# Performance work log

Hardware: AMD Instinct MI355X
Metric: run time of the kernel (lower is better)

Reference implementation:

```python
import jax, jax.numpy as jnp
import numpy as np

TEMPERATURE = 0.04


def _d3tod2(t):
    # 'c h w -> (h w) c'
    c, h, w = t.shape
    return jnp.transpose(t, (1, 2, 0)).reshape(h * w, c)


def setup_inputs() -> dict:
    key = jax.random.key(0)
    k1, k2 = jax.random.split(key)
    B, C, H, W = 4, 128, 96, 96
    # scale 0.05 keeps dot/temperature in a numerically sane range for exp
    x = jax.random.normal(k1, (B, C, H, W), dtype=jnp.float32) * 0.05
    label = jax.random.randint(k2, (B, 1, H, W), 0, 3, dtype=jnp.int32)
    return {"x": x, "label": label}


def reference(x, label):
    B, C, H, W = x.shape
    hw = H * W
    feat_1 = _d3tod2(x[0])                     # [HW, C]
    feat_2 = _d3tod2(x[1])                     # [HW, C]
    gt1 = label[0, 0].reshape(hw)              # [HW]
    gt2 = label[1, 0].reshape(hw)              # [HW]
    sim = jnp.exp(jnp.matmul(feat_1, feat_2.T) / TEMPERATURE)  # [HW, HW]
    mask = gt1[:, None] == gt2[None, :]        # [HW, HW] label-equality
    pos_sum = jnp.sum(jnp.where(mask, sim, jnp.zeros((), sim.dtype)))
    total_sum = jnp.sum(sim)
    loss = -jnp.log(pos_sum / total_sum) / (hw * hw)
    return loss
```

## Files before the change

kernel.cpp:

```cpp
#include <hip/hip_runtime.h>
#include <hip/hip_bf16.h>

#define HW 9216
#define CDIM 128
#define BM 128
#define BN 64
#define JT 8
#define GRID_I (HW / BM)
#define GRID_J (HW / (BN * JT))
#define NPART (GRID_I * GRID_J * 4)
#define LDP (CDIM + 8)

using bf16 = __hip_bfloat16;
typedef __attribute__((ext_vector_type(4))) float f32x4;
typedef __attribute__((ext_vector_type(8))) short s16x8;

#define EXP_SCALE 36.067376022224085f

#if __has_builtin(__builtin_amdgcn_exp2f)
#define FEXP2(x) __builtin_amdgcn_exp2f(x)
#else
#define FEXP2(x) exp2f(x)
#endif

__global__ __launch_bounds__(256) void prep_kernel(const float* __restrict__ x,
                                                   bf16* __restrict__ feat) {
    __shared__ float tile[64][65];
    const float* xs = x + (size_t)blockIdx.z * CDIM * HW;
    bf16* fs = feat + (size_t)blockIdx.z * HW * CDIM;
    float scale = (blockIdx.z == 0) ? EXP_SCALE : 1.0f;

    int p0 = blockIdx.x * 64;
    int c0 = blockIdx.y * 64;
    int t  = threadIdx.x;

    int pc = t & 63;
    int cr = t >> 6;
#pragma unroll
    for (int i = 0; i < 16; ++i) {
        int cl = cr + i * 4;
        tile[cl][pc] = xs[(size_t)(c0 + cl) * HW + p0 + pc];
    }
    __syncthreads();

    int cc = t & 63;
    int pr = t >> 6;
#pragma unroll
    for (int i = 0; i < 16; ++i) {
        int pl = pr + i * 4;
        fs[(size_t)(p0 + pl) * CDIM + c0 + cc] = __float2bfloat16(tile[cc][pl] * scale);
    }
}

__global__ __launch_bounds__(256) void simsum_kernel(const bf16* __restrict__ feat1,
                                                     const bf16* __restrict__ feat2,
                                                     const int* __restrict__ label,
                                                     float* __restrict__ partials) {
    __shared__ bf16 Bs[2][BN][LDP];
    __shared__ int  labs[JT * BN];
    __shared__ float red[8];

    int t    = threadIdx.x;
    int w    = t >> 6;
    int lane = t & 63;
    int lr   = lane & 15;
    int kg   = lane >> 4;

    int i0 = blockIdx.x * BM;
    int jb = blockIdx.y * (JT * BN);

    s16x8 af[2][4];
#pragma unroll
    for (int m = 0; m < 2; ++m) {
        const bf16* arow = &feat1[(size_t)(i0 + w * 32 + m * 16 + lr) * CDIM + kg * 8];
#pragma unroll
        for (int ks = 0; ks < 4; ++ks)
            af[m][ks] = *(const s16x8*)(arow + ks * 32);
    }

    int g1v[2][4];
#pragma unroll
    for (int m = 0; m < 2; ++m)
#pragma unroll
        for (int r2 = 0; r2 < 4; ++r2)
            g1v[m][r2] = label[i0 + w * 32 + m * 16 + kg * 4 + r2];

    const int* lab2 = label + HW;
    {
        int la = lab2[jb + t];
        int lb = lab2[jb + 256 + t];
        labs[t]       = la;
        labs[t + 256] = lb;
    }

    int srow = t >> 4;
    int sch8 = (t & 15) * 8;
    s16x8 rb[4];

    auto load_tile = [&](int tt) {
#pragma unroll
        for (int q = 0; q < 4; ++q)
            rb[q] = *(const s16x8*)(&feat2[(size_t)(jb + tt * BN + srow + q * 16) * CDIM + sch8]);
    };
    auto write_tile = [&](int bsel) {
#pragma unroll
        for (int q = 0; q < 4; ++q)
            *(s16x8*)(&Bs[bsel][srow + q * 16][sch8]) = rb[q];
    };

    load_tile(0);  write_tile(0);
    load_tile(1);  write_tile(1);
    load_tile(2);
    asm volatile("s_waitcnt lgkmcnt(0)" ::: "memory");
    __builtin_amdgcn_sched_barrier(0);
    __builtin_amdgcn_s_barrier();

    float tot0 = 0.f, tot1 = 0.f, pos0 = 0.f, pos1 = 0.f;

#pragma unroll
    for (int tt = 0; tt < JT; ++tt) {
        int g2v[4];
#pragma unroll
        for (int n = 0; n < 4; ++n)
            g2v[n] = labs[tt * BN + n * 16 + lr];

        f32x4 acc[2][4] = {};
#pragma unroll
        for (int ks = 0; ks < 4; ++ks) {
            int kbase = ks * 32 + kg * 8;
            s16x8 bfv[4];
#pragma unroll
            for (int n = 0; n < 4; ++n)
                bfv[n] = *(const s16x8*)(&Bs[tt & 1][n * 16 + lr][kbase]);
#pragma unroll
            for (int m = 0; m < 2; ++m)
#pragma unroll
                for (int n = 0; n < 4; ++n)
                    acc[m][n] = __builtin_amdgcn_mfma_f32_16x16x32_bf16(af[m][ks], bfv[n], acc[m][n], 0, 0, 0);
        }

        __builtin_amdgcn_sched_barrier(0);
        __builtin_amdgcn_s_barrier();

        if (tt + 2 < JT) write_tile(tt & 1);
        if (tt + 3 < JT) load_tile(tt + 3);

#pragma unroll
        for (int n = 0; n < 4; ++n) {
#pragma unroll
            for (int r2 = 0; r2 < 4; ++r2) {
                float e0 = FEXP2(acc[0][n][r2]);
                tot0 += e0;
                pos0 += (g1v[0][r2] == g2v[n]) ? e0 : 0.f;
                float e1 = FEXP2(acc[1][n][r2]);
                tot1 += e1;
                pos1 += (g1v[1][r2] == g2v[n]) ? e1 : 0.f;
            }
        }

        if (tt + 1 < JT) {
            asm volatile("s_waitcnt lgkmcnt(0)" ::: "memory");
            __builtin_amdgcn_sched_barrier(0);
            __builtin_amdgcn_s_barrier();
        }
    }

    float tot = tot0 + tot1, pos = pos0 + pos1;
#pragma unroll
    for (int off = 32; off; off >>= 1) {
        tot += __shfl_down(tot, off);
        pos += __shfl_down(pos, off);
    }
    if (lane == 0) { red[w * 2] = tot; red[w * 2 + 1] = pos; }
    __syncthreads();
    if (t == 0) {
        float T4 = red[0] + red[2] + red[4] + red[6];
        float P4 = red[1] + red[3] + red[5] + red[7];
        int bid = blockIdx.y * GRID_I + blockIdx.x;
        partials[(bid * 4 + 0) * 2] = T4;
        partials[(bid * 4 + 0) * 2 + 1] = P4;
        partials[(bid * 4 + 1) * 2] = 0.f; partials[(bid * 4 + 1) * 2 + 1] = 0.f;
        partials[(bid * 4 + 2) * 2] = 0.f; partials[(bid * 4 + 2) * 2 + 1] = 0.f;
        partials[(bid * 4 + 3) * 2] = 0.f; partials[(bid * 4 + 3) * 2 + 1] = 0.f;
    }
}

__global__ __launch_bounds__(256) void finalize_kernel(const float* __restrict__ partials,
                                                       float* __restrict__ out) {
    double tot = 0.0, pos = 0.0;
    int t = threadIdx.x;
    for (int i = t; i < NPART; i += 256) {
        tot += (double)partials[i * 2];
        pos += (double)partials[i * 2 + 1];
    }
#pragma unroll
    for (int off = 32; off; off >>= 1) {
        tot += __shfl_down(tot, off);
        pos += __shfl_down(pos, off);
    }
    __shared__ double rt[4], rp[4];
    int w = t >> 6, lane = t & 63;
    if (lane == 0) { rt[w] = tot; rp[w] = pos; }
    __syncthreads();
    if (t == 0) {
        double T = rt[0] + rt[1] + rt[2] + rt[3];
        double P = rp[0] + rp[1] + rp[2] + rp[3];
        double hw2 = (double)HW * (double)HW;
        out[0] = (float)(-log(P / T) / hw2);
    }
}

extern "C" void kernel_launch(void* const* d_in, const int* in_sizes, int n_in,
                              void* d_out, int out_size, void* d_ws, size_t ws_size,
                              hipStream_t stream) {
    const float* x     = (const float*)d_in[0];
    const int*   label = (const int*)d_in[1];
    float*       out   = (float*)d_out;

    bf16*  feat  = (bf16*)d_ws;
    float* parts = (float*)((char*)d_ws + 2 * (size_t)HW * CDIM * sizeof(bf16));

    dim3 g1(HW / 64, CDIM / 64, 2);
    prep_kernel<<<g1, 256, 0, stream>>>(x, feat);

    dim3 g2(GRID_I, GRID_J);
    simsum_kernel<<<g2, 256, 0, stream>>>(feat, feat + (size_t)HW * CDIM, label, parts);

    finalize_kernel<<<1, 256, 0, stream>>>(parts, out);
}
```

Measured before the change: 51.17 us.

## Switch similarity GEMM to 32x32x16 MFMA with 512-thread blocks

Replaces the 16x16x32 bf16 MFMA tiling with 32x32x16 MFMA, so each wave covers 32 rows by 64 columns, and doubles the block to 512 threads with BM=256 and JT=4. Column labels are now read directly from global memory rather than staged in shared memory, and only one partial per block is written. The aim is fewer LDS B-fragment reads per FLOP and higher MFMA throughput. In exchange the grid has fewer, larger blocks, register pressure rises from the 16-wide accumulators, and the shorter JT gives the three-stage load pipeline less work to overlap.

```diff
diff --git a/kernel.cpp b/kernel.cpp
--- a/kernel.cpp
+++ b/kernel.cpp
@@ -3,16 +3,16 @@
 
 #define HW 9216
 #define CDIM 128
-#define BM 128
+#define BM 256
 #define BN 64
-#define JT 8
+#define JT 4
 #define GRID_I (HW / BM)
 #define GRID_J (HW / (BN * JT))
-#define NPART (GRID_I * GRID_J * 4)
+#define NPART (GRID_I * GRID_J)
 #define LDP (CDIM + 8)
 
 using bf16 = __hip_bfloat16;
-typedef __attribute__((ext_vector_type(4))) float f32x4;
+typedef __attribute__((ext_vector_type(16))) float f32x16;
 typedef __attribute__((ext_vector_type(8))) short s16x8;
 
 #define EXP_SCALE 36.067376022224085f
@@ -52,60 +52,48 @@
     }
 }
 
-__global__ __launch_bounds__(256) void simsum_kernel(const bf16* __restrict__ feat1,
-                                                     const bf16* __restrict__ feat2,
-                                                     const int* __restrict__ label,
-                                                     float* __restrict__ partials) {
+__global__ __launch_bounds__(512, 4) void simsum_kernel(const bf16* __restrict__ feat1,
+                                                        const bf16* __restrict__ feat2,
+                                                        const int* __restrict__ label,
+                                                        float* __restrict__ partials) {
     __shared__ bf16 Bs[2][BN][LDP];
-    __shared__ int  labs[JT * BN];
-    __shared__ float red[8];
+    __shared__ float red[16];
 
     int t    = threadIdx.x;
     int w    = t >> 6;
     int lane = t & 63;
-    int lr   = lane & 15;
-    int kg   = lane >> 4;
-
-    int i0 = blockIdx.x * BM;
-    int jb = blockIdx.y * (JT * BN);
-
-    s16x8 af[2][4];
-#pragma unroll
-    for (int m = 0; m < 2; ++m) {
-        const bf16* arow = &feat1[(size_t)(i0 + w * 32 + m * 16 + lr) * CDIM + kg * 8];
-#pragma unroll
-        for (int ks = 0; ks < 4; ++ks)
-            af[m][ks] = *(const s16x8*)(arow + ks * 32);
-    }
-
-    int g1v[2][4];
-#pragma unroll
-    for (int m = 0; m < 2; ++m)
-#pragma unroll
-        for (int r2 = 0; r2 < 4; ++r2)
-            g1v[m][r2] = label[i0 + w * 32 + m * 16 + kg * 4 + r2];
-
-    const int* lab2 = label + HW;
+    int cl   = lane & 31;
+    int hi   = lane >> 5;
+
+    int i0  = blockIdx.x * BM;
+    int jb  = blockIdx.y * (BN * JT);
+    int r0w = i0 + w * 32;
+
+    s16x8 af[8];
     {
-        int la = lab2[jb + t];
-        int lb = lab2[jb + 256 + t];
-        labs[t]       = la;
-        labs[t + 256] = lb;
-    }
+        const bf16* arow = &feat1[(size_t)(r0w + cl) * CDIM + hi * 8];
+#pragma unroll
+        for (int s = 0; s < 8; ++s)
+            af[s] = *(const s16x8*)(arow + s * 16);
+    }
+
+    int4 g1i[4];
+#pragma unroll
+    for (int q = 0; q < 4; ++q)
+        g1i[q] = *(const int4*)(&label[r0w + 4 * hi + 8 * q]);
 
     int srow = t >> 4;
     int sch8 = (t & 15) * 8;
-    s16x8 rb[4];
+    s16x8 rb[2];
 
     auto load_tile = [&](int tt) {
-#pragma unroll
-        for (int q = 0; q < 4; ++q)
-            rb[q] = *(const s16x8*)(&feat2[(size_t)(jb + tt * BN + srow + q * 16) * CDIM + sch8]);
+        const bf16* base = &feat2[(size_t)(jb + tt * BN + srow) * CDIM + sch8];
+        rb[0] = *(const s16x8*)(base);
+        rb[1] = *(const s16x8*)(base + 32 * CDIM);
     };
-    auto write_tile = [&](int bsel) {
-#pragma unroll
-        for (int q = 0; q < 4; ++q)
-            *(s16x8*)(&Bs[bsel][srow + q * 16][sch8]) = rb[q];
+    auto write_tile = [&](int b) {
+        *(s16x8*)(&Bs[b][srow][sch8])      = rb[0];
+        *(s16x8*)(&Bs[b][srow + 32][sch8]) = rb[1];
     };
 
     load_tile(0);  write_tile(0);
@@ -115,28 +103,22 @@
     __builtin_amdgcn_sched_barrier(0);
     __builtin_amdgcn_s_barrier();
 
+    const int* lab2 = label + HW;
     float tot0 = 0.f, tot1 = 0.f, pos0 = 0.f, pos1 = 0.f;
 
 #pragma unroll
     for (int tt = 0; tt < JT; ++tt) {
-        int g2v[4];
-#pragma unroll
-        for (int n = 0; n < 4; ++n)
-            g2v[n] = labs[tt * BN + n * 16 + lr];
-
-        f32x4 acc[2][4] = {};
-#pragma unroll
-        for (int ks = 0; ks < 4; ++ks) {
-            int kbase = ks * 32 + kg * 8;
-            s16x8 bfv[4];
-#pragma unroll
-            for (int n = 0; n < 4; ++n)
-                bfv[n] = *(const s16x8*)(&Bs[tt & 1][n * 16 + lr][kbase]);
-#pragma unroll
-            for (int m = 0; m < 2; ++m)
-#pragma unroll
-                for (int n = 0; n < 4; ++n)
-                    acc[m][n] = __builtin_amdgcn_mfma_f32_16x16x32_bf16(af[m][ks], bfv[n], acc[m][n], 0, 0, 0);
+        int g2a = lab2[jb + tt * BN + cl];
+        int g2b = lab2[jb + tt * BN + 32 + cl];
+
+        f32x16 acc0 = {}, acc1 = {};
+#pragma unroll
+        for (int s = 0; s < 8; ++s) {
+            const bf16* bp = &Bs[tt & 1][cl][s * 16 + hi * 8];
+            s16x8 b0 = *(const s16x8*)(bp);
+            s16x8 b1 = *(const s16x8*)(bp + (size_t)32 * LDP);
+            acc0 = __builtin_amdgcn_mfma_f32_32x32x16_bf16(af[s], b0, acc0, 0, 0, 0);
+            acc1 = __builtin_amdgcn_mfma_f32_32x32x16_bf16(af[s], b1, acc1, 0, 0, 0);
         }
 
         __builtin_amdgcn_sched_barrier(0);
@@ -146,16 +128,14 @@
         if (tt + 3 < JT) load_tile(tt + 3);
 
 #pragma unroll
-        for (int n = 0; n < 4; ++n) {
-#pragma unroll
-            for (int r2 = 0; r2 < 4; ++r2) {
-                float e0 = FEXP2(acc[0][n][r2]);
-                tot0 += e0;
-                pos0 += (g1v[0][r2] == g2v[n]) ? e0 : 0.f;
-                float e1 = FEXP2(acc[1][n][r2]);
-                tot1 += e1;
-                pos1 += (g1v[1][r2] == g2v[n]) ? e1 : 0.f;
-            }
+        for (int r = 0; r < 16; ++r) {
+            int g1 = ((const int*)g1i)[r];
+            float e0 = FEXP2(acc0[r]);
+            tot0 += e0;
+            pos0 += (g1 == g2a) ? e0 : 0.f;
+            float e1 = FEXP2(acc1[r]);
+            tot1 += e1;
+            pos1 += (g1 == g2b) ? e1 : 0.f;
         }
 
         if (tt + 1 < JT) {
@@ -174,14 +154,12 @@
     if (lane == 0) { red[w * 2] = tot; red[w * 2 + 1] = pos; }
     __syncthreads();
     if (t == 0) {
-        float T4 = red[0] + red[2] + red[4] + red[6];
-        float P4 = red[1] + red[3] + red[5] + red[7];
+        float T = 0.f, P = 0.f;
+#pragma unroll
+        for (int q = 0; q < 8; ++q) { T += red[q * 2]; P += red[q * 2 + 1]; }
         int bid = blockIdx.y * GRID_I + blockIdx.x;
-        partials[(bid * 4 + 0) * 2] = T4;
-        partials[(bid * 4 + 0) * 2 + 1] = P4;
-        partials[(bid * 4 + 1) * 2] = 0.f; partials[(bid * 4 + 1) * 2 + 1] = 0.f;
-        partials[(bid * 4 + 2) * 2] = 0.f; partials[(bid * 4 + 2) * 2 + 1] = 0.f;
-        partials[(bid * 4 + 3) * 2] = 0.f; partials[(bid * 4 + 3) * 2 + 1] = 0.f;
+        partials[bid * 2]     = T;
+        partials[bid * 2 + 1] = P;
     }
 }
 
@@ -224,7 +202,7 @@
     prep_kernel<<<g1, 256, 0, stream>>>(x, feat);
 
     dim3 g2(GRID_I, GRID_J);
-    simsum_kernel<<<g2, 256, 0, stream>>>(feat, feat + (size_t)HW * CDIM, label, parts);
+    simsum_kernel<<<g2, 512, 0, stream>>>(feat, feat + (size_t)HW * CDIM, label, parts);
 
     finalize_kernel<<<1, 256, 0, stream>>>(parts, out);
 }
```

After: 50.55 us. No clear change (-1.2%).
